# Optimization experiments

Measured on AMD Instinct MI355X. Metric: run time of the kernel, lower is better.

The kernel has to match this reference:

```python
import jax, jax.numpy as jnp
import numpy as np

N, F, H, C, HX, E = 50000, 256, 128, 16, 64, 500000
TEMP = 1.0


def gcn_conv(x, src, dst, W, b, n):
    # PyG GCNConv: x @ W, add self-loops, sym-normalized scatter-sum src->dst
    xw = x @ W
    idx = jnp.arange(n)
    s = jnp.concatenate([src, idx])
    d = jnp.concatenate([dst, idx])
    deg = jax.ops.segment_sum(jnp.ones_like(s, dtype=xw.dtype), d, num_segments=n)
    dinv = jnp.where(deg > 0, jax.lax.rsqrt(deg), 0.0)
    norm = dinv[s] * dinv[d]
    out = jax.ops.segment_sum(xw[s] * norm[:, None], d, num_segments=n)
    return out + b


def setup_inputs() -> dict:
    key = jax.random.key(0)
    ks = jax.random.split(key, 16)
    x = jax.random.normal(ks[0], (N, F), jnp.float32)
    edge_index = jax.random.randint(ks[1], (2, E), 0, N)
    neg_edge_index = jax.random.randint(ks[2], (2, E), 0, N)
    y = jax.random.randint(ks[3], (N,), 0, C)
    train_mask = jax.random.uniform(ks[4], (N,)) < 0.5
    def lin(k, fi, fo):
        s = 1.0 / np.sqrt(fi)
        return jax.random.uniform(k, (fi, fo), jnp.float32, -s, s)
    W1 = lin(ks[5], F, H); b1 = jnp.zeros((H,), jnp.float32)
    W2 = lin(ks[6], H, C); b2 = jnp.zeros((C,), jnp.float32)
    Wx = lin(ks[7], F, HX); bx = jnp.zeros((HX,), jnp.float32)
    Wd = lin(ks[8], 2 * (HX + C), 1); bd = jnp.zeros((1,), jnp.float32)
    return dict(x=x, edge_index=edge_index, neg_edge_index=neg_edge_index, y=y,
                train_mask=train_mask, W1=W1, b1=b1, W2=W2, b2=b2,
                Wx=Wx, bx=bx, Wd=Wd, bd=bd)


def reference(x, edge_index, neg_edge_index, y, train_mask,
              W1, b1, W2, b2, Wx, bx, Wd, bd):
    n = x.shape[0]
    # GNN encoder p(y|x,G): 2-layer GCN (eval mode -> dropout identity)
    h = jax.nn.relu(gcn_conv(x, edge_index[0], edge_index[1], W1, b1, n))
    logits = gcn_conv(h, edge_index[0], edge_index[1], W2, b2, n) / TEMP
    y_log_prob = jax.nn.log_softmax(logits, axis=-1)
    y_prob = jnp.where(train_mask[:, None],
                       jax.nn.one_hot(y, logits.shape[-1], dtype=logits.dtype),
                       jnp.exp(y_log_prob))
    # node feature encoder
    xe = jax.nn.relu(x @ Wx + bx)
    def decode(ei):
        s, d = ei[0], ei[1]
        feat = jnp.concatenate([xe[s], xe[d], y_prob[s], y_prob[d]], axis=1)
        return feat @ Wd + bd
    e_pred_pos = decode(edge_index)
    e_pred_neg = decode(neg_edge_index)
    return e_pred_pos, e_pred_neg, y_log_prob
```

## Files before the change

kernel.cpp:

```cpp
#include <hip/hip_runtime.h>

typedef unsigned short ushort_t;
typedef __attribute__((ext_vector_type(8))) short short8;
typedef __attribute__((ext_vector_type(4))) float floatx4;

constexpr int F = 256, H = 128, C = 16, HX = 64;
constexpr int NBCOL = H + HX;

__device__ __forceinline__ ushort_t f2bf(float f) {
  unsigned u = __float_as_uint(f);
  u += 0x7fffu + ((u >> 16) & 1u);
  return (ushort_t)(u >> 16);
}
__device__ __forceinline__ float bflo(unsigned u) { return __uint_as_float(u << 16); }
__device__ __forceinline__ float bfhi(unsigned u) { return __uint_as_float(u & 0xffff0000u); }

__global__ void k_pre(const float* __restrict__ x, ushort_t* __restrict__ xb, int totalU,
                      const float* __restrict__ W1, const float* __restrict__ Wx,
                      ushort_t* __restrict__ WBt,
                      const int* __restrict__ dst, int* __restrict__ deg, int e,
                      int n, int nbx, int nbw) {
  int b = blockIdx.x;
  if (b < nbx) {
    int i = b * 256 + threadIdx.x;
    if (i >= totalU) return;
    int tile = i >> 9, rem = i & 511, j = rem >> 4, l15 = rem & 15;
    int row = tile * 16 + l15;
    ushort4 lo = make_ushort4(0, 0, 0, 0), hi = lo;
    if (row < n) {
      const float4* xp = (const float4*)(x + (size_t)row * F + j * 8);
      float4 a = xp[0], bb = xp[1];
      lo = make_ushort4(f2bf(a.x), f2bf(a.y), f2bf(a.z), f2bf(a.w));
      hi = make_ushort4(f2bf(bb.x), f2bf(bb.y), f2bf(bb.z), f2bf(bb.w));
    }
    ((ushort4*)xb)[2 * i] = lo;
    ((ushort4*)xb)[2 * i + 1] = hi;
  } else if (b < nbx + nbw) {
    int i = (b - nbx) * 256 + threadIdx.x;
    if (i >= NBCOL * F) return;
    int nn = i / F, k = i % F;
    float v = (nn < H) ? W1[k * H + nn] : Wx[k * HX + (nn - H)];
    WBt[nn * F + k] = f2bf(v);
  } else {
    int i = (b - nbx - nbw) * 256 + threadIdx.x;
    if (i < e) atomicAdd(&deg[dst[i]], 1);
  }
}

__global__ void k_scan_a(const int* __restrict__ deg, int* __restrict__ part, int n) {
  __shared__ int sm[256];
  int i = blockIdx.x * 256 + threadIdx.x;
  int v = (i < n) ? deg[i] : 0;
  sm[threadIdx.x] = v;
  __syncthreads();
  for (int s = 128; s > 0; s >>= 1) {
    if (threadIdx.x < s) sm[threadIdx.x] += sm[threadIdx.x + s];
    __syncthreads();
  }
  if (threadIdx.x == 0) part[blockIdx.x] = sm[0];
}

__global__ void k_scan_c(const int* __restrict__ deg, const int* __restrict__ part,
                         int* __restrict__ row_start, int* __restrict__ cursor,
                         float* __restrict__ dinv, int n, int e) {
  __shared__ int psm[256];
  __shared__ int wsum[4], woff[4];
  int c = blockIdx.x, t = threadIdx.x;
  psm[t] = (t < c) ? part[t] : 0;
  __syncthreads();
  for (int s = 128; s > 0; s >>= 1) {
    if (t < s) psm[t] += psm[t + s];
    __syncthreads();
  }
  int blockoff = psm[0];
  __syncthreads();

  int i = c * 256 + t;
  int lane = t & 63, wid = t >> 6;
  int v = (i < n) ? deg[i] : 0;
  int xs = v;
  for (int d = 1; d < 64; d <<= 1) {
    int u = __shfl_up(xs, d);
    if (lane >= d) xs += u;
  }
  if (lane == 63) wsum[wid] = xs;
  __syncthreads();
  if (t == 0) {
    int s = 0;
    for (int w = 0; w < 4; w++) { woff[w] = s; s += wsum[w]; }
  }
  __syncthreads();
  int excl = xs - v + woff[wid] + blockoff;
  if (i < n) {
    row_start[i] = excl;
    cursor[i] = excl;
    dinv[i] = rsqrtf((float)(v + 1));
  }
  if (i == 0) row_start[n] = e;
}

__global__ void k_fill(const int* __restrict__ src, const int* __restrict__ dst,
                       const float* __restrict__ dinv, int* __restrict__ cursor,
                       int2* __restrict__ csr8, int e) {
  int i = blockIdx.x * 256 + threadIdx.x;
  if (i < e) {
    int s = src[i];
    int p = atomicAdd(&cursor[dst[i]], 1);
    csr8[p] = make_int2(s, __float_as_int(dinv[s]));
  }
}

__global__ __launch_bounds__(256, 3) void k_gemm1(const ushort_t* __restrict__ xb,
                                                  const ushort_t* __restrict__ WBt,
                                                  const float* __restrict__ bx,
                                                  ushort_t* __restrict__ xw1,
                                                  float* __restrict__ xe,
                                                  int n, int ntiles) {
  int w = threadIdx.x >> 6, lane = threadIdx.x & 63;
  int q = lane >> 4, l15 = lane & 15;
  const short8* bb = (const short8*)WBt;
  short8 bfr[3][8];
#pragma unroll
  for (int t = 0; t < 3; t++)
#pragma unroll
    for (int kk = 0; kk < 8; kk++)
      bfr[t][kk] = bb[(size_t)(w * 48 + t * 16 + l15) * 32 + kk * 4 + q];

  float bxv[3];
#pragma unroll
  for (int t = 0; t < 3; t++) {
    int g = w * 48 + t * 16;
    bxv[t] = (g >= H) ? bx[g - H + l15] : 0.0f;
  }

  const short8* ab = (const short8*)xb;
  for (int tile = blockIdx.x; tile < ntiles; tile += gridDim.x) {
    const short8* atile = ab + (size_t)tile * 512;
    short8 a[8];
#pragma unroll
    for (int kk = 0; kk < 8; kk++) a[kk] = atile[kk * 64 + q * 16 + l15];

    floatx4 acc0 = (floatx4)(0.0f), acc1 = (floatx4)(0.0f), acc2 = (floatx4)(0.0f);
#pragma unroll
    for (int kk = 0; kk < 8; kk++) {
      acc0 = __builtin_amdgcn_mfma_f32_16x16x32_bf16(a[kk], bfr[0][kk], acc0, 0, 0, 0);
      acc1 = __builtin_amdgcn_mfma_f32_16x16x32_bf16(a[kk], bfr[1][kk], acc1, 0, 0, 0);
      acc2 = __builtin_amdgcn_mfma_f32_16x16x32_bf16(a[kk], bfr[2][kk], acc2, 0, 0, 0);
    }

    floatx4 accs[3] = {acc0, acc1, acc2};
    int rbase = tile * 16 + q * 4;
#pragma unroll
    for (int t = 0; t < 3; t++) {
      int g = w * 48 + t * 16;
#pragma unroll
      for (int r = 0; r < 4; r++) {
        int ro = rbase + r;
        if (ro < n) {
          if (g < H) {
            xw1[(size_t)ro * H + g + l15] = f2bf(accs[t][r]);
          } else {
            xe[(size_t)ro * HX + (g - H) + l15] = fmaxf(accs[t][r] + bxv[t], 0.0f);
          }
        }
      }
    }
  }
}

__global__ void k_agg1g2(const ushort_t* __restrict__ xw1, const int* __restrict__ row_start,
                         const int2* __restrict__ csr8, const float* __restrict__ dinv,
                         const float* __restrict__ b1, const float* __restrict__ W2,
                         float* __restrict__ hw2, int n) {
  __shared__ float2 hsm[4][64];
  int wid = threadIdx.x >> 6;
  int v = blockIdx.x * 4 + wid;
  if (v >= n) return;
  int lane = threadIdx.x & 63;
  float dv = dinv[v];
  unsigned sv = ((const unsigned*)(xw1 + (size_t)v * H))[lane];
  float ax = dv * bflo(sv), ay = dv * bfhi(sv);
  int j0 = row_start[v], j1 = row_start[v + 1];
  int j = j0;
  for (; j + 8 <= j1; j += 8) {
    int2 ee[8];
    unsigned rr[8];
#pragma unroll
    for (int u = 0; u < 8; u++) ee[u] = csr8[j + u];
#pragma unroll
    for (int u = 0; u < 8; u++)
      rr[u] = ((const unsigned*)(xw1 + (size_t)ee[u].x * H))[lane];
#pragma unroll
    for (int u = 0; u < 8; u++) {
      float wu = __int_as_float(ee[u].y);
      ax += wu * bflo(rr[u]);
      ay += wu * bfhi(rr[u]);
    }
  }
  for (; j < j1; j++) {
    int2 e0 = csr8[j];
    unsigned r0 = ((const unsigned*)(xw1 + (size_t)e0.x * H))[lane];
    float w0 = __int_as_float(e0.y);
    ax += w0 * bflo(r0);
    ay += w0 * bfhi(r0);
  }
  int c2 = lane * 2;
  float o0 = fmaxf(dv * ax + b1[c2], 0.0f);
  float o1 = fmaxf(dv * ay + b1[c2 + 1], 0.0f);
  hsm[wid][lane] = make_float2(o0, o1);

  int c = lane & 15, g = lane >> 4;
  const float* hrow = (const float*)hsm[wid];
  float p = 0.0f;
#pragma unroll
  for (int jj = 0; jj < 32; jj++)
    p += hrow[g * 32 + jj] * W2[(g * 32 + jj) * C + c];
  p += __shfl_xor(p, 16);
  p += __shfl_xor(p, 32);
  if (g == 0) hw2[(size_t)v * C + c] = p;
}

__global__ void k_agg2ab(const float* __restrict__ hw2, const int* __restrict__ row_start,
                         const int2* __restrict__ csr8, const float* __restrict__ dinv,
                         const float* __restrict__ b2, const int* __restrict__ y,
                         const int* __restrict__ tmask, const float* __restrict__ xe,
                         const float* __restrict__ Wd, float* __restrict__ ylp_out,
                         float* __restrict__ Aarr, float* __restrict__ Barr, int n) {
  int idx = blockIdx.x * 256 + threadIdx.x;
  int node = idx >> 4, c = idx & 15;
  if (node >= n) return;
  float dv = dinv[node];
  float acc = dv * hw2[(size_t)node * C + c];
  int j0 = row_start[node], j1 = row_start[node + 1];
  int j = j0;
  for (; j + 8 <= j1; j += 8) {
    int2 ee[8];
    float rr[8];
#pragma unroll
    for (int u = 0; u < 8; u++) ee[u] = csr8[j + u];
#pragma unroll
    for (int u = 0; u < 8; u++) rr[u] = hw2[(size_t)ee[u].x * C + c];
#pragma unroll
    for (int u = 0; u < 8; u++) acc += __int_as_float(ee[u].y) * rr[u];
  }
  for (; j + 4 <= j1; j += 4) {
    int2 e0 = csr8[j], e1 = csr8[j + 1], e2 = csr8[j + 2], e3 = csr8[j + 3];
    float r0 = hw2[(size_t)e0.x * C + c];
    float r1 = hw2[(size_t)e1.x * C + c];
    float r2 = hw2[(size_t)e2.x * C + c];
    float r3 = hw2[(size_t)e3.x * C + c];
    acc += __int_as_float(e0.y) * r0 + __int_as_float(e1.y) * r1 +
           __int_as_float(e2.y) * r2 + __int_as_float(e3.y) * r3;
  }
  for (; j < j1; j++) {
    int2 e0 = csr8[j];
    acc += __int_as_float(e0.y) * hw2[(size_t)e0.x * C + c];
  }
  float logit = dv * acc + b2[c];
  float m = logit;
  for (int o = 8; o > 0; o >>= 1) m = fmaxf(m, __shfl_xor(m, o, 16));
  float e = expf(logit - m);
  float s16 = e;
  for (int o = 8; o > 0; o >>= 1) s16 += __shfl_xor(s16, o, 16);
  float lp = (logit - m) - logf(s16);
  ylp_out[(size_t)node * C + c] = lp;
  float yp = tmask[node] ? ((y[node] == c) ? 1.0f : 0.0f) : (e / s16);

  float4 xv = *(const float4*)(xe + (size_t)node * HX + c * 4);
  float4 wa = *(const float4*)(Wd + c * 4);
  float4 wb = *(const float4*)(Wd + HX + c * 4);
  float pa = xv.x * wa.x + xv.y * wa.y + xv.z * wa.z + xv.w * wa.w + yp * Wd[2 * HX + c];
  float pb = xv.x * wb.x + xv.y * wb.y + xv.z * wb.z + xv.w * wb.w + yp * Wd[2 * HX + C + c];
  for (int o = 8; o > 0; o >>= 1) {
    pa += __shfl_xor(pa, o, 16);
    pb += __shfl_xor(pb, o, 16);
  }
  if (c == 0) { Aarr[node] = pa; Barr[node] = pb; }
}

__global__ void k_decode(const int* __restrict__ ei, const int* __restrict__ nei,
                         const float* __restrict__ Aarr, const float* __restrict__ Barr,
                         const float* __restrict__ bd, float* __restrict__ out, int e) {
  int i = blockIdx.x * 256 + threadIdx.x;
  if (i >= 2 * e) return;
  float b0 = bd[0];
  if (i < e) {
    int s = ei[i], d = ei[e + i];
    out[i] = Aarr[s] + Barr[d] + b0;
  } else {
    int j = i - e;
    int s = nei[j], d = nei[e + j];
    out[e + j] = Aarr[s] + Barr[d] + b0;
  }
}

extern "C" void kernel_launch(void* const* d_in, const int* in_sizes, int n_in,
                              void* d_out, int out_size, void* d_ws, size_t ws_size,
                              hipStream_t stream) {
  const float* x = (const float*)d_in[0];
  const int* ei = (const int*)d_in[1];
  const int* nei = (const int*)d_in[2];
  const int* y = (const int*)d_in[3];
  const int* tmask = (const int*)d_in[4];
  const float* W1 = (const float*)d_in[5];
  const float* b1 = (const float*)d_in[6];
  const float* W2 = (const float*)d_in[7];
  const float* b2 = (const float*)d_in[8];
  const float* Wx = (const float*)d_in[9];
  const float* bx = (const float*)d_in[10];
  const float* Wd = (const float*)d_in[11];
  const float* bd = (const float*)d_in[12];
  float* out = (float*)d_out;

  int n = in_sizes[3];
  int e = in_sizes[1] / 2;
  int ntiles = (n + 15) / 16;

  char* ws = (char*)d_ws;
  size_t off = 0;
  auto alloc = [&](size_t bytes) -> void* {
    void* p = ws + off;
    off += (bytes + 511) & ~(size_t)511;
    return p;
  };
  int* deg = (int*)alloc((size_t)n * 4);
  ushort_t* xb = (ushort_t*)alloc((size_t)ntiles * 16 * F * 2);
  ushort_t* WBt = (ushort_t*)alloc((size_t)NBCOL * F * 2);
  ushort_t* xw1 = (ushort_t*)alloc((size_t)n * H * 2);
  float* xe = (float*)alloc((size_t)n * HX * 4);
  float* hw2 = (float*)alloc((size_t)n * C * 4);
  float* dinv = (float*)alloc((size_t)n * 4);
  int* row_start = (int*)alloc((size_t)(n + 1) * 4);
  int* cursor = (int*)alloc((size_t)n * 4);
  int2* csr8 = (int2*)alloc((size_t)e * 8);
  int* part = (int*)alloc(1024 * 4);
  float* Aarr = (float*)alloc((size_t)n * 4);
  float* Barr = (float*)alloc((size_t)n * 4);

  const int* src = ei;
  const int* dst = ei + e;

  hipMemsetAsync(deg, 0, (size_t)n * 4, stream);

  int totalU = ntiles * 512;
  int nbx = (totalU + 255) / 256;
  int nbw = (NBCOL * F + 255) / 256;
  int nbe = (e + 255) / 256;
  k_pre<<<nbx + nbw + nbe, 256, 0, stream>>>(x, xb, totalU, W1, Wx, WBt, dst, deg, e,
                                             n, nbx, nbw);

  int nchunk = (n + 255) / 256;
  k_scan_a<<<nchunk, 256, 0, stream>>>(deg, part, n);
  k_scan_c<<<nchunk, 256, 0, stream>>>(deg, part, row_start, cursor, dinv, n, e);
  k_fill<<<(e + 255) / 256, 256, 0, stream>>>(src, dst, dinv, cursor, csr8, e);

  int ggrid = ntiles < 768 ? ntiles : 768;
  k_gemm1<<<ggrid, 256, 0, stream>>>(xb, WBt, bx, xw1, xe, n, ntiles);
  k_agg1g2<<<(n + 3) / 4, 256, 0, stream>>>(xw1, row_start, csr8, dinv, b1, W2, hw2, n);
  k_agg2ab<<<(n * 16 + 255) / 256, 256, 0, stream>>>(hw2, row_start, csr8, dinv, b2, y,
                                                     tmask, xe, Wd, out + (size_t)2 * e,
                                                     Aarr, Barr, n);
  k_decode<<<(2 * e + 255) / 256, 256, 0, stream>>>(ei, nei, Aarr, Barr, bd, out, e);
}
```

Baseline: 251.7 us.

## Split layer-1 aggregation into column strips with partial W2 products

The xw1 buffer is now written in four 32-column strips, each stored contiguously per node, and the layer-1 aggregation runs one strip per block. Within a wave, four edges are processed in parallel by 16-lane groups and then reduced with shuffles. Each strip computes a partial h·W2 product into a separate buffer, and a new small kernel sums the four partials. The goal is better cache locality, since each strip's working set is a quarter of the full xw1. In exchange the CSR indices are read four times, there is an extra kernel launch, and a partial buffer must be written and read back.

```diff
diff --git a/kernel.cpp b/kernel.cpp
--- a/kernel.cpp
+++ b/kernel.cpp
@@ -158,7 +158,9 @@
         int ro = rbase + r;
         if (ro < n) {
           if (g < H) {
-            xw1[(size_t)ro * H + g + l15] = f2bf(accs[t][r]);
+            int strip = g >> 5;
+            int half = g & 16;
+            xw1[((size_t)strip * n + ro) * 32 + half + l15] = f2bf(accs[t][r]);
           } else {
             xe[(size_t)ro * HX + (g - H) + l15] = fmaxf(accs[t][r] + bxv[t], 0.0f);
           }
@@ -168,56 +170,64 @@
   }
 }
 
-__global__ void k_agg1g2(const ushort_t* __restrict__ xw1, const int* __restrict__ row_start,
-                         const int2* __restrict__ csr8, const float* __restrict__ dinv,
-                         const float* __restrict__ b1, const float* __restrict__ W2,
-                         float* __restrict__ hw2, int n) {
-  __shared__ float2 hsm[4][64];
-  int wid = threadIdx.x >> 6;
-  int v = blockIdx.x * 4 + wid;
+__global__ void k_agg1s(const ushort_t* __restrict__ xw1s, const int* __restrict__ row_start,
+                        const int2* __restrict__ csr8, const float* __restrict__ dinv,
+                        const float* __restrict__ b1, const float* __restrict__ W2,
+                        float* __restrict__ hw2p, int n) {
+  __shared__ float hsm[4][32];
+  int wid = threadIdx.x >> 6, lane = threadIdx.x & 63;
+  int strip = blockIdx.x & 3;
+  int v = (blockIdx.x >> 2) * 4 + wid;
   if (v >= n) return;
-  int lane = threadIdx.x & 63;
+  int eu = lane >> 4, cp = lane & 15;
   float dv = dinv[v];
-  unsigned sv = ((const unsigned*)(xw1 + (size_t)v * H))[lane];
-  float ax = dv * bflo(sv), ay = dv * bfhi(sv);
+  const unsigned* xs = (const unsigned*)xw1s + (size_t)strip * n * 16;
+  unsigned sv = xs[(size_t)v * 16 + cp];
   int j0 = row_start[v], j1 = row_start[v + 1];
+  float ax = 0.0f, ay = 0.0f;
   int j = j0;
   for (; j + 8 <= j1; j += 8) {
-    int2 ee[8];
-    unsigned rr[8];
-#pragma unroll
-    for (int u = 0; u < 8; u++) ee[u] = csr8[j + u];
-#pragma unroll
-    for (int u = 0; u < 8; u++)
-      rr[u] = ((const unsigned*)(xw1 + (size_t)ee[u].x * H))[lane];
-#pragma unroll
-    for (int u = 0; u < 8; u++) {
-      float wu = __int_as_float(ee[u].y);
-      ax += wu * bflo(rr[u]);
-      ay += wu * bfhi(rr[u]);
+    int2 e0 = csr8[j + eu], e1 = csr8[j + 4 + eu];
+    unsigned r0 = xs[(size_t)e0.x * 16 + cp];
+    unsigned r1 = xs[(size_t)e1.x * 16 + cp];
+    float w0 = __int_as_float(e0.y), w1 = __int_as_float(e1.y);
+    ax += w0 * bflo(r0) + w1 * bflo(r1);
+    ay += w0 * bfhi(r0) + w1 * bfhi(r1);
+  }
+  for (; j < j1; j += 4) {
+    int je = j + eu;
+    if (je < j1) {
+      int2 e0 = csr8[je];
+      unsigned r0 = xs[(size_t)e0.x * 16 + cp];
+      float w0 = __int_as_float(e0.y);
+      ax += w0 * bflo(r0);
+      ay += w0 * bfhi(r0);
     }
   }
-  for (; j < j1; j++) {
-    int2 e0 = csr8[j];
-    unsigned r0 = ((const unsigned*)(xw1 + (size_t)e0.x * H))[lane];
-    float w0 = __int_as_float(e0.y);
-    ax += w0 * bflo(r0);
-    ay += w0 * bfhi(r0);
-  }
-  int c2 = lane * 2;
-  float o0 = fmaxf(dv * ax + b1[c2], 0.0f);
-  float o1 = fmaxf(dv * ay + b1[c2 + 1], 0.0f);
-  hsm[wid][lane] = make_float2(o0, o1);
-
-  int c = lane & 15, g = lane >> 4;
-  const float* hrow = (const float*)hsm[wid];
+  ax += __shfl_xor(ax, 16); ay += __shfl_xor(ay, 16);
+  ax += __shfl_xor(ax, 32); ay += __shfl_xor(ay, 32);
+  float o0 = fmaxf(dv * (ax + dv * bflo(sv)) + b1[strip * 32 + cp * 2], 0.0f);
+  float o1 = fmaxf(dv * (ay + dv * bfhi(sv)) + b1[strip * 32 + cp * 2 + 1], 0.0f);
+  if (eu == 0) hsm[wid][cp * 2] = o0, hsm[wid][cp * 2 + 1] = o1;
+
+  int c = cp, kh = eu;
+  const float* hrow = hsm[wid];
   float p = 0.0f;
 #pragma unroll
-  for (int jj = 0; jj < 32; jj++)
-    p += hrow[g * 32 + jj] * W2[(g * 32 + jj) * C + c];
+  for (int jj = 0; jj < 8; jj++)
+    p += hrow[kh * 8 + jj] * W2[(strip * 32 + kh * 8 + jj) * C + c];
   p += __shfl_xor(p, 16);
   p += __shfl_xor(p, 32);
-  if (g == 0) hw2[(size_t)v * C + c] = p;
+  if (kh == 0) hw2p[((size_t)strip * n + v) * C + c] = p;
+}
+
+__global__ void k_sum4(const float* __restrict__ hw2p, float* __restrict__ hw2, int n) {
+  int i = blockIdx.x * 256 + threadIdx.x;
+  int tot = n * C;
+  if (i < tot) {
+    size_t s = (size_t)n * C;
+    hw2[i] = hw2p[i] + hw2p[i + s] + hw2p[i + 2 * s] + hw2p[i + 3 * s];
+  }
 }
 
 __global__ void k_agg2ab(const float* __restrict__ hw2, const int* __restrict__ row_start,
@@ -329,6 +339,7 @@
   ushort_t* xw1 = (ushort_t*)alloc((size_t)n * H * 2);
   float* xe = (float*)alloc((size_t)n * HX * 4);
   float* hw2 = (float*)alloc((size_t)n * C * 4);
+  float* hw2p = (float*)alloc((size_t)4 * n * C * 4);
   float* dinv = (float*)alloc((size_t)n * 4);
   int* row_start = (int*)alloc((size_t)(n + 1) * 4);
   int* cursor = (int*)alloc((size_t)n * 4);
@@ -356,7 +367,9 @@
 
   int ggrid = ntiles < 768 ? ntiles : 768;
   k_gemm1<<<ggrid, 256, 0, stream>>>(xb, WBt, bx, xw1, xe, n, ntiles);
-  k_agg1g2<<<(n + 3) / 4, 256, 0, stream>>>(xw1, row_start, csr8, dinv, b1, W2, hw2, n);
+  k_agg1s<<<((n + 3) / 4) * 4, 256, 0, stream>>>(xw1, row_start, csr8, dinv, b1, W2,
+                                                 hw2p, n);
+  k_sum4<<<(n * C + 255) / 256, 256, 0, stream>>>(hw2p, hw2, n);
   k_agg2ab<<<(n * 16 + 255) / 256, 256, 0, stream>>>(hw2, row_start, csr8, dinv, b2, y,
                                                      tmask, xe, Wd, out + (size_t)2 * e,
                                                      Aarr, Barr, n);
```

Result: slower. 292.7 us (+16.3%).
